# Kernel optimization log

Hardware: AMD Instinct MI355X
Metric: run time of the kernel (lower is better)

The kernel has to match this reference:

```python
import jax, jax.numpy as jnp
import numpy as np

HIDDEN = 1024
TILE = 128


def setup_inputs() -> dict:
    key = jax.random.key(0)
    ks = jax.random.split(key, 9)
    B, S, D = 2, 4096, HIDDEN
    s = 1.0 / np.sqrt(D)
    return {
        "batch": jax.random.normal(ks[0], (B, S, D), jnp.float32),
        "Wq": jax.random.normal(ks[1], (D, D), jnp.float32) * s,
        "bq": jax.random.normal(ks[2], (D,), jnp.float32) * 0.01,
        "Wk": jax.random.normal(ks[3], (D, D), jnp.float32) * s,
        "bk": jax.random.normal(ks[4], (D,), jnp.float32) * 0.01,
        "Wv": jax.random.normal(ks[5], (D, D), jnp.float32) * s,
        "bv": jax.random.normal(ks[6], (D,), jnp.float32) * 0.01,
        "Wo": jax.random.normal(ks[7], (D, D), jnp.float32) * s,
        "bo": jax.random.normal(ks[8], (D,), jnp.float32) * 0.01,
    }


def reference(batch, Wq, bq, Wk, bk, Wv, bv, Wo, bo):
    B, S, D = batch.shape
    scale = 1.0 / np.sqrt(D)
    T = S // TILE  # seq_len chosen divisible by tile size

    # Projections (nn.Linear: x @ W.T + b)
    q = batch @ Wq.T + bq
    k = batch @ Wk.T + bk
    v = batch @ Wv.T + bv

    # Tile K/V along the sequence axis: [B, T, TILE, D]
    k_t = k.reshape(B, T, TILE, D)
    v_t = v.reshape(B, T, TILE, D)

    # Per-tile scores and per-tile softmax (NOT a global softmax —
    # faithful to the module, which normalizes within each kv tile).
    scores = jnp.einsum("bqd,btkd->btqk", q, k_t) * scale  # [B, T, S, TILE]
    w = jax.nn.softmax(scores, axis=-1)

    # Sum of per-tile attention outputs over kv tiles
    out = jnp.einsum("btqk,btkd->bqd", w, v_t)  # [B, S, D]

    # Normalizing factor: sum of per-tile softmax weights (== T analytically,
    # computed explicitly to match the original math bit-for-bit in spirit)
    norm = w.sum(axis=-1).sum(axis=1)[..., None]  # [B, S, 1]
    out = out / (norm + 1e-6)

    return out @ Wo.T + bo
```

## Files before the change

kernel.cpp:

```cpp
#include <hip/hip_runtime.h>


#define D_ 1024
#define S_ 4096
#define B_ 2

typedef unsigned short u16;
typedef float f32x4 __attribute__((ext_vector_type(4)));
typedef float float4v __attribute__((ext_vector_type(4)));
typedef __bf16 bf16x8 __attribute__((ext_vector_type(8)));
typedef unsigned short us8 __attribute__((ext_vector_type(8)));

static __device__ __forceinline__ u16 f2bf(float f) {
    unsigned int u = __builtin_bit_cast(unsigned int, f);
    u += 0x7FFFu + ((u >> 16) & 1u);
    return (u16)(u >> 16);
}

static __device__ __forceinline__ void gld16(const u16* g, u16* l) {
    __builtin_amdgcn_global_load_lds(
        (const __attribute__((address_space(1))) void*)g,
        (__attribute__((address_space(3))) void*)l, 16, 0, 0);
}

static __device__ __forceinline__ void xcd_map(int& bx, int& by) {
    const int gx = gridDim.x, gy = gridDim.y;
    int lin = blockIdx.x + blockIdx.y * gx;
    int ry = gy >> 3;
    int idx = lin >> 3;
    int q = idx / ry;
    bx = q;
    by = (lin & 7) * ry + (idx - q * ry);
}

__global__ void cast_kernel(const float* __restrict__ in, u16* __restrict__ out, int n8) {
    int i = blockIdx.x * blockDim.x + threadIdx.x;
    int stride = gridDim.x * blockDim.x;
    for (; i < n8; i += stride) {
        const float4v* p = (const float4v*)in + 2 * (size_t)i;
        float4v a = p[0], b = p[1];
        us8 o;
        o[0] = f2bf(a[0]); o[1] = f2bf(a[1]); o[2] = f2bf(a[2]); o[3] = f2bf(a[3]);
        o[4] = f2bf(b[0]); o[5] = f2bf(b[1]); o[6] = f2bf(b[2]); o[7] = f2bf(b[3]);
        *((us8*)out + i) = o;
    }
}

__global__ void cast4_kernel(const float* __restrict__ w0, const float* __restrict__ w1,
                             const float* __restrict__ w2, const float* __restrict__ w3,
                             u16* __restrict__ out, int n8per) {
    const float* srcs[4] = {w0, w1, w2, w3};
    const float* in = srcs[blockIdx.y];
    u16* o = out + (size_t)blockIdx.y * (size_t)n8per * 8;
    int i = blockIdx.x * blockDim.x + threadIdx.x;
    int stride = gridDim.x * blockDim.x;
    for (; i < n8per; i += stride) {
        const float4v* p = (const float4v*)in + 2 * (size_t)i;
        float4v a = p[0], b = p[1];
        us8 v;
        v[0] = f2bf(a[0]); v[1] = f2bf(a[1]); v[2] = f2bf(a[2]); v[3] = f2bf(a[3]);
        v[4] = f2bf(b[0]); v[5] = f2bf(b[1]); v[6] = f2bf(b[2]); v[7] = f2bf(b[3]);
        *((us8*)o + i) = v;
    }
}

__global__ void concat_bias(const float* __restrict__ b0, const float* __restrict__ b1,
                            const float* __restrict__ b2, float* __restrict__ out) {
    int i = blockIdx.x * 256 + threadIdx.x;
    const float* s = (i < 1024) ? b0 : ((i < 2048) ? b1 : b2);
    out[i] = s[i & 1023];
}

__global__ void transpose_v(const u16* __restrict__ V, u16* __restrict__ Vt, int ldv) {
    __shared__ u16 t[64][72];
    const int tid = threadIdx.x;
    const int d0 = blockIdx.x * 64;
    const int s0 = blockIdx.y * 64;
    const u16* Vb = V + (size_t)blockIdx.z * ((size_t)S_ * ldv);
    u16* Vtb = Vt + (size_t)blockIdx.z * ((size_t)D_ * S_);
#pragma unroll
    for (int it = 0; it < 2; it++) {
        int idx = it * 256 + tid;
        int row = idx >> 3;
        int ch = idx & 7;
        us8 v = *(const us8*)&Vb[(size_t)(s0 + row) * ldv + d0 + ch * 8];
        *(us8*)&t[row][ch * 8] = v;
    }
    __syncthreads();
#pragma unroll
    for (int it = 0; it < 2; it++) {
        int idx = it * 256 + tid;
        int jj = idx >> 3;
        int ch = idx & 7;
        us8 v;
#pragma unroll
        for (int e = 0; e < 8; e++) v[e] = t[ch * 8 + e][jj];
        *(us8*)&Vtb[(size_t)(d0 + jj) * S_ + s0 + ch * 8] = v;
    }
}

template <int EPI>
__global__ __launch_bounds__(256, 2) void gemm_bt(
    const u16* __restrict__ A, const u16* __restrict__ B, void* __restrict__ Cv,
    const float* __restrict__ bias, int K, int lda, int ldb, int ldc,
    long sA, long sB, long sC, float scale)
{
    __shared__ u16 lA[128 * 32];
    __shared__ u16 lB[128 * 32];
    const int tid = threadIdx.x;
    const int lane = tid & 63;
    const int wid = tid >> 6;
    const int wr = wid >> 1, wc = wid & 1;
    const int z = blockIdx.z;
    A += (size_t)z * sA;
    B += (size_t)z * sB;
    int bx, by;
    xcd_map(bx, by);
    const int m0 = by * 128;
    const int n0 = bx * 128;

    f32x4 acc[4][4];
#pragma unroll
    for (int i = 0; i < 4; i++)
#pragma unroll
        for (int j = 0; j < 4; j++)
#pragma unroll
            for (int r = 0; r < 4; r++) acc[i][j][r] = 0.0f;

    const int ar = lane & 15;
    const int ak = (lane >> 4) * 8;
    const int srow = tid >> 2;
    const int scol = (tid & 3) * 8;
    const u16* ga = A + (size_t)(m0 + srow) * lda + scol;
    const u16* gb = B + (size_t)(n0 + srow) * ldb + scol;

    for (int k0 = 0; k0 < K; k0 += 32) {
        gld16(ga + k0, &lA[tid * 8]);
        gld16(ga + k0 + (size_t)64 * lda, &lA[2048 + tid * 8]);
        gld16(gb + k0, &lB[tid * 8]);
        gld16(gb + k0 + (size_t)64 * ldb, &lB[2048 + tid * 8]);
        __syncthreads();
        bf16x8 afr[4], bfr[4];
#pragma unroll
        for (int mi = 0; mi < 4; mi++)
            afr[mi] = *(const bf16x8*)&lA[(wr * 64 + mi * 16 + ar) * 32 + ak];
#pragma unroll
        for (int ni = 0; ni < 4; ni++)
            bfr[ni] = *(const bf16x8*)&lB[(wc * 64 + ni * 16 + ar) * 32 + ak];
#pragma unroll
        for (int mi = 0; mi < 4; mi++)
#pragma unroll
            for (int ni = 0; ni < 4; ni++)
                acc[mi][ni] = __builtin_amdgcn_mfma_f32_16x16x32_bf16(
                    afr[mi], bfr[ni], acc[mi][ni], 0, 0, 0);
        __syncthreads();
    }

    const int rr = (lane >> 4) * 4;
    const int cc = lane & 15;
#pragma unroll
    for (int mi = 0; mi < 4; mi++) {
#pragma unroll
        for (int ni = 0; ni < 4; ni++) {
            const int col = n0 + wc * 64 + ni * 16 + cc;
            const int rowb = m0 + wr * 64 + mi * 16 + rr;
            if constexpr (EPI == 0) {
                u16* C = (u16*)Cv + (size_t)z * sC;
                const float bv = bias[col];
#pragma unroll
                for (int r = 0; r < 4; r++)
                    C[(size_t)(rowb + r) * ldc + col] = f2bf(acc[mi][ni][r] + bv);
            } else if constexpr (EPI == 1) {
                u16* C = (u16*)Cv + (size_t)z * sC;
#pragma unroll
                for (int r = 0; r < 4; r++)
                    C[(size_t)(rowb + r) * ldc + col] = f2bf(acc[mi][ni][r] * scale);
            } else {
                float* C = (float*)Cv + (size_t)z * sC;
                const float bv = bias[col];
#pragma unroll
                for (int r = 0; r < 4; r++)
                    C[(size_t)(rowb + r) * ldc + col] = acc[mi][ni][r] + bv;
            }
        }
    }
}

__global__ __launch_bounds__(256, 2) void gemm_scores(
    const u16* __restrict__ Q, const u16* __restrict__ Kmat, u16* __restrict__ W,
    int K, int lda, int ldb, int ldc, long sQ, long sK, long sW)
{
    __shared__ u16 lA[128 * 32];
    __shared__ u16 lB[128 * 32];
    const int tid = threadIdx.x;
    const int lane = tid & 63;
    const int wid = tid >> 6;
    const int z = blockIdx.z;
    const u16* Aq = Q + (size_t)z * sQ;
    const u16* Bk = Kmat + (size_t)z * sK;
    int bx, by;
    xcd_map(bx, by);
    const int m0 = by * 128;
    const int n0 = bx * 128;

    f32x4 acc[2][8];
#pragma unroll
    for (int i = 0; i < 2; i++)
#pragma unroll
        for (int j = 0; j < 8; j++)
#pragma unroll
            for (int r = 0; r < 4; r++) acc[i][j][r] = 0.0f;

    const int ar = lane & 15;
    const int ak = (lane >> 4) * 8;
    const int srow = tid >> 2;
    const int scol = (tid & 3) * 8;
    const u16* ga = Aq + (size_t)(m0 + srow) * lda + scol;
    const u16* gb = Bk + (size_t)(n0 + srow) * ldb + scol;

    for (int k0 = 0; k0 < K; k0 += 32) {
        gld16(ga + k0, &lA[tid * 8]);
        gld16(ga + k0 + (size_t)64 * lda, &lA[2048 + tid * 8]);
        gld16(gb + k0, &lB[tid * 8]);
        gld16(gb + k0 + (size_t)64 * ldb, &lB[2048 + tid * 8]);
        __syncthreads();
        bf16x8 afr[2], bfr[8];
#pragma unroll
        for (int mi = 0; mi < 2; mi++)
            afr[mi] = *(const bf16x8*)&lA[(wid * 32 + mi * 16 + ar) * 32 + ak];
#pragma unroll
        for (int ni = 0; ni < 8; ni++)
            bfr[ni] = *(const bf16x8*)&lB[(ni * 16 + ar) * 32 + ak];
#pragma unroll
        for (int mi = 0; mi < 2; mi++)
#pragma unroll
            for (int ni = 0; ni < 8; ni++)
                acc[mi][ni] = __builtin_amdgcn_mfma_f32_16x16x32_bf16(
                    afr[mi], bfr[ni], acc[mi][ni], 0, 0, 0);
        __syncthreads();
    }

    const float SL = 0.03125f * 1.44269504088896341f;
    const int g4 = (lane >> 4) * 4;
    const int cc = lane & 15;
    u16* Wp = W + (size_t)z * sW;
#pragma unroll
    for (int mi = 0; mi < 2; mi++) {
#pragma unroll
        for (int r = 0; r < 4; r++) {
            float m = acc[mi][0][r];
#pragma unroll
            for (int ni = 1; ni < 8; ni++) m = fmaxf(m, acc[mi][ni][r]);
            m = fmaxf(m, __shfl_xor(m, 1));
            m = fmaxf(m, __shfl_xor(m, 2));
            m = fmaxf(m, __shfl_xor(m, 4));
            m = fmaxf(m, __shfl_xor(m, 8));
            float e[8], s = 0.0f;
#pragma unroll
            for (int ni = 0; ni < 8; ni++) {
                e[ni] = exp2f((acc[mi][ni][r] - m) * SL);
                s += e[ni];
            }
            s += __shfl_xor(s, 1);
            s += __shfl_xor(s, 2);
            s += __shfl_xor(s, 4);
            s += __shfl_xor(s, 8);
            const float inv = 1.0f / s;
            const int row = m0 + wid * 32 + mi * 16 + g4 + r;
#pragma unroll
            for (int ni = 0; ni < 8; ni++)
                Wp[(size_t)row * ldc + n0 + ni * 16 + cc] = f2bf(e[ni] * inv);
        }
    }
}

extern "C" void kernel_launch(void* const* d_in, const int* in_sizes, int n_in,
                              void* d_out, int out_size, void* d_ws, size_t ws_size,
                              hipStream_t stream)
{
    const float* X  = (const float*)d_in[0];
    const float* Wq = (const float*)d_in[1];
    const float* bq = (const float*)d_in[2];
    const float* Wk = (const float*)d_in[3];
    const float* bk = (const float*)d_in[4];
    const float* Wv = (const float*)d_in[5];
    const float* bv = (const float*)d_in[6];
    const float* Wo = (const float*)d_in[7];
    const float* bo = (const float*)d_in[8];
    float* OUT = (float*)d_out;

    u16* ws = (u16*)d_ws;
    const size_t NTOK = (size_t)B_ * S_;
    const size_t XSZ = NTOK * D_;
    u16* Xb   = ws;
    u16* QKVb = Xb + XSZ;
    u16* Vt   = QKVb + NTOK * (size_t)(3 * D_);
    u16* Wqb  = Vt + XSZ;
    u16* Wsm  = Wqb + (size_t)4 * D_ * D_;
    float* bqkv = (float*)(Wsm + (size_t)B_ * S_ * S_);
    u16* Ob   = Xb;

    u16* Qp = QKVb;
    u16* Kp = QKVb + D_;
    u16* Vp = QKVb + 2 * D_;
    const int ldqkv = 3 * D_;

    cast_kernel<<<dim3(2048), dim3(256), 0, stream>>>(X, Xb, (int)(XSZ / 8));
    cast4_kernel<<<dim3(512, 4), dim3(256), 0, stream>>>(Wq, Wk, Wv, Wo, Wqb,
                                                         (int)((size_t)D_ * D_ / 8));
    concat_bias<<<dim3(12), dim3(256), 0, stream>>>(bq, bk, bv, bqkv);

    gemm_bt<0><<<dim3(3 * D_ / 128, NTOK / 128, 1), 256, 0, stream>>>(
        Xb, Wqb, QKVb, bqkv, D_, D_, D_, ldqkv, 0, 0, 0, 1.0f);

    transpose_v<<<dim3(D_ / 64, S_ / 64, B_), 256, 0, stream>>>(Vp, Vt, ldqkv);

    gemm_scores<<<dim3(S_ / 128, S_ / 128, B_), 256, 0, stream>>>(
        Qp, Kp, Wsm, D_, ldqkv, ldqkv, S_,
        (long)S_ * ldqkv, (long)S_ * ldqkv, (long)S_ * S_);

    gemm_bt<1><<<dim3(D_ / 128, S_ / 128, B_), 256, 0, stream>>>(
        Wsm, Vt, Ob, nullptr, S_, S_, S_, D_,
        (long)S_ * S_, (long)D_ * S_, (long)S_ * D_, 1.0f / (32.0f + 1e-6f));

    gemm_bt<2><<<dim3(D_ / 128, NTOK / 128, 1), 256, 0, stream>>>(
        Ob, Wqb + (size_t)3 * D_ * D_, OUT, bo, D_, D_, D_, D_, 0, 0, 0, 1.0f);
}
```

Before: 405.1 us.

## Replace GEMMs with 8-wave 256-wide tiles using a 4-stage async LDS pipeline

All GEMMs move onto one templated kernel with 512 threads, 256-column output tiles and a 4-deep ring of LDS buffers. Global-to-LDS loads are issued three k-steps ahead and gated by explicit vmcnt waits instead of full __syncthreads. The kernel also XOR-swizzles the LDS layout to avoid bank conflicts and raises wave priority around the MFMA blocks. The score GEMM now uses 256x256 tiles, so the per-128-column softmax reduces across wave pairs through shared memory. The larger LDS footprint and one block per CU reduce occupancy, and the hand-tuned waitcnt counts make correctness depend on the exact number of outstanding loads.

After: 406.4 us. No clear change (+0.3%).

```diff
diff --git a/kernel.cpp b/kernel.cpp
--- a/kernel.cpp
+++ b/kernel.cpp
@@ -21,6 +21,15 @@
     __builtin_amdgcn_global_load_lds(
         (const __attribute__((address_space(1))) void*)g,
         (__attribute__((address_space(3))) void*)l, 16, 0, 0);
+}
+
+template <int N>
+static __device__ __forceinline__ void waitv() {
+    if constexpr (N == 0)      asm volatile("s_waitcnt vmcnt(0)" ::: "memory");
+    else if constexpr (N == 3) asm volatile("s_waitcnt vmcnt(3)" ::: "memory");
+    else if constexpr (N == 4) asm volatile("s_waitcnt vmcnt(4)" ::: "memory");
+    else if constexpr (N == 6) asm volatile("s_waitcnt vmcnt(6)" ::: "memory");
+    else if constexpr (N == 8) asm volatile("s_waitcnt vmcnt(8)" ::: "memory");
 }
 
 static __device__ __forceinline__ void xcd_map(int& bx, int& by) {
@@ -99,177 +108,203 @@
     }
 }
 
-template <int EPI>
-__global__ __launch_bounds__(256, 2) void gemm_bt(
+template <int BM, int EPI>
+__global__ __launch_bounds__(512, 1) void gemm8(
     const u16* __restrict__ A, const u16* __restrict__ B, void* __restrict__ Cv,
     const float* __restrict__ bias, int K, int lda, int ldb, int ldc,
     long sA, long sB, long sC, float scale)
 {
-    __shared__ u16 lA[128 * 32];
-    __shared__ u16 lB[128 * 32];
+    constexpr int MI = BM / 32;
+    constexpr int MH = MI / 2;
+    constexpr int LPT_A = BM / 128;
+    constexpr int LPT = LPT_A + 2;
+
+    __shared__ u16 lA[4][BM * 32];
+    __shared__ u16 lB[4][256 * 32];
+    __shared__ float sred[2][8][128];
+
     const int tid = threadIdx.x;
     const int lane = tid & 63;
     const int wid = tid >> 6;
-    const int wr = wid >> 1, wc = wid & 1;
+    const int wr = wid >> 2;
+    const int wc = wid & 3;
+    const int ar = lane & 15;
+    const int sl = lane >> 4;
     const int z = blockIdx.z;
     A += (size_t)z * sA;
     B += (size_t)z * sB;
     int bx, by;
     xcd_map(bx, by);
-    const int m0 = by * 128;
-    const int n0 = bx * 128;
-
-    f32x4 acc[4][4];
-#pragma unroll
-    for (int i = 0; i < 4; i++)
+    const int m0 = by * BM;
+    const int n0 = bx * 256;
+    const int NT = K >> 5;
+
+    f32x4 acc[MI][4];
+#pragma unroll
+    for (int i = 0; i < MI; i++)
 #pragma unroll
         for (int j = 0; j < 4; j++)
 #pragma unroll
             for (int r = 0; r < 4; r++) acc[i][j][r] = 0.0f;
 
-    const int ar = lane & 15;
-    const int ak = (lane >> 4) * 8;
-    const int srow = tid >> 2;
-    const int scol = (tid & 3) * 8;
-    const u16* ga = A + (size_t)(m0 + srow) * lda + scol;
-    const u16* gb = B + (size_t)(n0 + srow) * ldb + scol;
-
-    for (int k0 = 0; k0 < K; k0 += 32) {
-        gld16(ga + k0, &lA[tid * 8]);
-        gld16(ga + k0 + (size_t)64 * lda, &lA[2048 + tid * 8]);
-        gld16(gb + k0, &lB[tid * 8]);
-        gld16(gb + k0 + (size_t)64 * ldb, &lB[2048 + tid * 8]);
-        __syncthreads();
-        bf16x8 afr[4], bfr[4];
-#pragma unroll
-        for (int mi = 0; mi < 4; mi++)
-            afr[mi] = *(const bf16x8*)&lA[(wr * 64 + mi * 16 + ar) * 32 + ak];
-#pragma unroll
-        for (int ni = 0; ni < 4; ni++)
-            bfr[ni] = *(const bf16x8*)&lB[(wc * 64 + ni * 16 + ar) * 32 + ak];
-#pragma unroll
-        for (int mi = 0; mi < 4; mi++)
+    auto stageA = [&](int t) {
+        const int k0 = t << 5;
+        u16* dst = &lA[t & 3][0];
+#pragma unroll
+        for (int j = 0; j < LPT_A; j++) {
+            int u = wid * (BM >> 1) + j * 64 + lane;
+            int row = u >> 2, ps = u & 3;
+            int ls = ps ^ ((row >> 1) & 3);
+            gld16(A + (size_t)(m0 + row) * lda + k0 + ls * 8, dst + u * 8);
+        }
+    };
+    auto stageB = [&](int t) {
+        const int k0 = t << 5;
+        u16* dst = &lB[t & 3][0];
+#pragma unroll
+        for (int j = 0; j < 2; j++) {
+            int u = wid * 128 + j * 64 + lane;
+            int row = u >> 2, ps = u & 3;
+            int ls = ps ^ ((row >> 1) & 3);
+            gld16(B + (size_t)(n0 + row) * ldb + k0 + ls * 8, dst + u * 8);
+        }
+    };
+    auto rdA = [&](int buf, int mi) -> bf16x8 {
+        int R = wr * (BM / 2) + mi * 16 + ar;
+        int ps = sl ^ ((R >> 1) & 3);
+        return *(const bf16x8*)&lA[buf][R * 32 + ps * 8];
+    };
+    auto rdB = [&](int buf, int ni) -> bf16x8 {
+        int R = wc * 64 + ni * 16 + ar;
+        int ps = sl ^ ((R >> 1) & 3);
+        return *(const bf16x8*)&lB[buf][R * 32 + ps * 8];
+    };
+
+    stageA(0); stageB(0);
+    stageA(1); stageB(1);
+    stageA(2); stageB(2);
+
+    for (int t = 0; t < NT; ++t) {
+        const int ahead = NT - 1 - t;
+        if (ahead >= 2)      waitv<2 * LPT>();
+        else if (ahead == 1) waitv<LPT>();
+        else                 waitv<0>();
+        __builtin_amdgcn_s_barrier();
+
+        const int buf = t & 3;
+        bf16x8 bfr[4];
+#pragma unroll
+        for (int ni = 0; ni < 4; ni++) bfr[ni] = rdB(buf, ni);
+        bf16x8 afr[MH];
+#pragma unroll
+        for (int mi = 0; mi < MH; mi++) afr[mi] = rdA(buf, mi);
+        if (t + 3 < NT) stageA(t + 3);
+        asm volatile("s_waitcnt lgkmcnt(0)" ::: "memory");
+        __builtin_amdgcn_sched_barrier(0);
+        __builtin_amdgcn_s_setprio(1);
+#pragma unroll
+        for (int mi = 0; mi < MH; mi++)
 #pragma unroll
             for (int ni = 0; ni < 4; ni++)
                 acc[mi][ni] = __builtin_amdgcn_mfma_f32_16x16x32_bf16(
                     afr[mi], bfr[ni], acc[mi][ni], 0, 0, 0);
+        __builtin_amdgcn_s_setprio(0);
+        __builtin_amdgcn_s_barrier();
+
+        bf16x8 afr2[MH];
+#pragma unroll
+        for (int mi = 0; mi < MH; mi++) afr2[mi] = rdA(buf, MH + mi);
+        if (t + 3 < NT) stageB(t + 3);
+        asm volatile("s_waitcnt lgkmcnt(0)" ::: "memory");
+        __builtin_amdgcn_sched_barrier(0);
+        __builtin_amdgcn_s_setprio(1);
+#pragma unroll
+        for (int mi = 0; mi < MH; mi++)
+#pragma unroll
+            for (int ni = 0; ni < 4; ni++)
+                acc[MH + mi][ni] = __builtin_amdgcn_mfma_f32_16x16x32_bf16(
+                    afr2[mi], bfr[ni], acc[MH + mi][ni], 0, 0, 0);
+        __builtin_amdgcn_s_setprio(0);
+    }
+
+    if constexpr (EPI == 3) {
+        const float SL = 0.03125f * 1.44269504088896341f;
+#pragma unroll
+        for (int mi = 0; mi < MI; mi++) {
+#pragma unroll
+            for (int r = 0; r < 4; r++) {
+                float m = acc[mi][0][r];
+#pragma unroll
+                for (int ni = 1; ni < 4; ni++) m = fmaxf(m, acc[mi][ni][r]);
+                m = fmaxf(m, __shfl_xor(m, 1));
+                m = fmaxf(m, __shfl_xor(m, 2));
+                m = fmaxf(m, __shfl_xor(m, 4));
+                m = fmaxf(m, __shfl_xor(m, 8));
+                if (ar == 0) sred[0][wid][mi * 16 + sl * 4 + r] = m;
+            }
+        }
         __syncthreads();
-    }
-
-    const int rr = (lane >> 4) * 4;
-    const int cc = lane & 15;
-#pragma unroll
-    for (int mi = 0; mi < 4; mi++) {
-#pragma unroll
-        for (int ni = 0; ni < 4; ni++) {
-            const int col = n0 + wc * 64 + ni * 16 + cc;
-            const int rowb = m0 + wr * 64 + mi * 16 + rr;
-            if constexpr (EPI == 0) {
-                u16* C = (u16*)Cv + (size_t)z * sC;
-                const float bv = bias[col];
-#pragma unroll
-                for (int r = 0; r < 4; r++)
-                    C[(size_t)(rowb + r) * ldc + col] = f2bf(acc[mi][ni][r] + bv);
-            } else if constexpr (EPI == 1) {
-                u16* C = (u16*)Cv + (size_t)z * sC;
-#pragma unroll
-                for (int r = 0; r < 4; r++)
-                    C[(size_t)(rowb + r) * ldc + col] = f2bf(acc[mi][ni][r] * scale);
-            } else {
-                float* C = (float*)Cv + (size_t)z * sC;
-                const float bv = bias[col];
-#pragma unroll
-                for (int r = 0; r < 4; r++)
-                    C[(size_t)(rowb + r) * ldc + col] = acc[mi][ni][r] + bv;
+#pragma unroll
+        for (int mi = 0; mi < MI; mi++) {
+#pragma unroll
+            for (int r = 0; r < 4; r++) {
+                const int rl = mi * 16 + sl * 4 + r;
+                const float mc = fmaxf(sred[0][wid][rl], sred[0][wid ^ 1][rl]);
+                float s = 0.0f;
+#pragma unroll
+                for (int ni = 0; ni < 4; ni++) {
+                    float e = exp2f((acc[mi][ni][r] - mc) * SL);
+                    acc[mi][ni][r] = e;
+                    s += e;
+                }
+                s += __shfl_xor(s, 1);
+                s += __shfl_xor(s, 2);
+                s += __shfl_xor(s, 4);
+                s += __shfl_xor(s, 8);
+                if (ar == 0) sred[1][wid][rl] = s;
             }
         }
-    }
-}
-
-__global__ __launch_bounds__(256, 2) void gemm_scores(
-    const u16* __restrict__ Q, const u16* __restrict__ Kmat, u16* __restrict__ W,
-    int K, int lda, int ldb, int ldc, long sQ, long sK, long sW)
-{
-    __shared__ u16 lA[128 * 32];
-    __shared__ u16 lB[128 * 32];
-    const int tid = threadIdx.x;
-    const int lane = tid & 63;
-    const int wid = tid >> 6;
-    const int z = blockIdx.z;
-    const u16* Aq = Q + (size_t)z * sQ;
-    const u16* Bk = Kmat + (size_t)z * sK;
-    int bx, by;
-    xcd_map(bx, by);
-    const int m0 = by * 128;
-    const int n0 = bx * 128;
-
-    f32x4 acc[2][8];
-#pragma unroll
-    for (int i = 0; i < 2; i++)
-#pragma unroll
-        for (int j = 0; j < 8; j++)
-#pragma unroll
-            for (int r = 0; r < 4; r++) acc[i][j][r] = 0.0f;
-
-    const int ar = lane & 15;
-    const int ak = (lane >> 4) * 8;
-    const int srow = tid >> 2;
-    const int scol = (tid & 3) * 8;
-    const u16* ga = Aq + (size_t)(m0 + srow) * lda + scol;
-    const u16* gb = Bk + (size_t)(n0 + srow) * ldb + scol;
-
-    for (int k0 = 0; k0 < K; k0 += 32) {
-        gld16(ga + k0, &lA[tid * 8]);
-        gld16(ga + k0 + (size_t)64 * lda, &lA[2048 + tid * 8]);
-        gld16(gb + k0, &lB[tid * 8]);
-        gld16(gb + k0 + (size_t)64 * ldb, &lB[2048 + tid * 8]);
         __syncthreads();
-        bf16x8 afr[2], bfr[8];
-#pragma unroll
-        for (int mi = 0; mi < 2; mi++)
-            afr[mi] = *(const bf16x8*)&lA[(wid * 32 + mi * 16 + ar) * 32 + ak];
-#pragma unroll
-        for (int ni = 0; ni < 8; ni++)
-            bfr[ni] = *(const bf16x8*)&lB[(ni * 16 + ar) * 32 + ak];
-#pragma unroll
-        for (int mi = 0; mi < 2; mi++)
-#pragma unroll
-            for (int ni = 0; ni < 8; ni++)
-                acc[mi][ni] = __builtin_amdgcn_mfma_f32_16x16x32_bf16(
-                    afr[mi], bfr[ni], acc[mi][ni], 0, 0, 0);
-        __syncthreads();
-    }
-
-    const float SL = 0.03125f * 1.44269504088896341f;
-    const int g4 = (lane >> 4) * 4;
-    const int cc = lane & 15;
-    u16* Wp = W + (size_t)z * sW;
-#pragma unroll
-    for (int mi = 0; mi < 2; mi++) {
-#pragma unroll
-        for (int r = 0; r < 4; r++) {
-            float m = acc[mi][0][r];
-#pragma unroll
-            for (int ni = 1; ni < 8; ni++) m = fmaxf(m, acc[mi][ni][r]);
-            m = fmaxf(m, __shfl_xor(m, 1));
-            m = fmaxf(m, __shfl_xor(m, 2));
-            m = fmaxf(m, __shfl_xor(m, 4));
-            m = fmaxf(m, __shfl_xor(m, 8));
-            float e[8], s = 0.0f;
-#pragma unroll
-            for (int ni = 0; ni < 8; ni++) {
-                e[ni] = exp2f((acc[mi][ni][r] - m) * SL);
-                s += e[ni];
+        u16* C = (u16*)Cv + (size_t)z * sC;
+#pragma unroll
+        for (int mi = 0; mi < MI; mi++) {
+#pragma unroll
+            for (int r = 0; r < 4; r++) {
+                const int rl = mi * 16 + sl * 4 + r;
+                const float inv = 1.0f / (sred[1][wid][rl] + sred[1][wid ^ 1][rl]);
+                const int row = m0 + wr * (BM / 2) + rl;
+#pragma unroll
+                for (int ni = 0; ni < 4; ni++)
+                    C[(size_t)row * ldc + n0 + wc * 64 + ni * 16 + ar] =
+                        f2bf(acc[mi][ni][r] * inv);
             }
-            s += __shfl_xor(s, 1);
-            s += __shfl_xor(s, 2);
-            s += __shfl_xor(s, 4);
-            s += __shfl_xor(s, 8);
-            const float inv = 1.0f / s;
-            const int row = m0 + wid * 32 + mi * 16 + g4 + r;
-#pragma unroll
-            for (int ni = 0; ni < 8; ni++)
-                Wp[(size_t)row * ldc + n0 + ni * 16 + cc] = f2bf(e[ni] * inv);
+        }
+    } else {
+#pragma unroll
+        for (int mi = 0; mi < MI; mi++) {
+#pragma unroll
+            for (int ni = 0; ni < 4; ni++) {
+                const int col = n0 + wc * 64 + ni * 16 + ar;
+                const int rowb = m0 + wr * (BM / 2) + mi * 16 + sl * 4;
+                if constexpr (EPI == 0) {
+                    u16* C = (u16*)Cv + (size_t)z * sC;
+                    const float bv = bias[col];
+#pragma unroll
+                    for (int r = 0; r < 4; r++)
+                        C[(size_t)(rowb + r) * ldc + col] = f2bf(acc[mi][ni][r] + bv);
+                } else if constexpr (EPI == 1) {
+                    u16* C = (u16*)Cv + (size_t)z * sC;
+#pragma unroll
+                    for (int r = 0; r < 4; r++)
+                        C[(size_t)(rowb + r) * ldc + col] = f2bf(acc[mi][ni][r] * scale);
+                } else {
+                    float* C = (float*)Cv + (size_t)z * sC;
+                    const float bv = bias[col];
+#pragma unroll
+                    for (int r = 0; r < 4; r++)
+                        C[(size_t)(rowb + r) * ldc + col] = acc[mi][ni][r] + bv;
+                }
+            }
         }
     }
 }
@@ -310,19 +345,19 @@
                                                          (int)((size_t)D_ * D_ / 8));
     concat_bias<<<dim3(12), dim3(256), 0, stream>>>(bq, bk, bv, bqkv);
 
-    gemm_bt<0><<<dim3(3 * D_ / 128, NTOK / 128, 1), 256, 0, stream>>>(
+    gemm8<128, 0><<<dim3(3 * D_ / 256, NTOK / 128, 1), 512, 0, stream>>>(
         Xb, Wqb, QKVb, bqkv, D_, D_, D_, ldqkv, 0, 0, 0, 1.0f);
 
     transpose_v<<<dim3(D_ / 64, S_ / 64, B_), 256, 0, stream>>>(Vp, Vt, ldqkv);
 
-    gemm_scores<<<dim3(S_ / 128, S_ / 128, B_), 256, 0, stream>>>(
-        Qp, Kp, Wsm, D_, ldqkv, ldqkv, S_,
-        (long)S_ * ldqkv, (long)S_ * ldqkv, (long)S_ * S_);
-
-    gemm_bt<1><<<dim3(D_ / 128, S_ / 128, B_), 256, 0, stream>>>(
+    gemm8<256, 3><<<dim3(S_ / 256, S_ / 256, B_), 512, 0, stream>>>(
+        Qp, Kp, Wsm, nullptr, D_, ldqkv, ldqkv, S_,
+        (long)S_ * ldqkv, (long)S_ * ldqkv, (long)S_ * S_, 1.0f);
+
+    gemm8<128, 1><<<dim3(D_ / 256, S_ / 128, B_), 512, 0, stream>>>(
         Wsm, Vt, Ob, nullptr, S_, S_, S_, D_,
         (long)S_ * S_, (long)D_ * S_, (long)S_ * D_, 1.0f / (32.0f + 1e-6f));
 
-    gemm_bt<2><<<dim3(D_ / 128, NTOK / 128, 1), 256, 0, stream>>>(
+    gemm8<128, 2><<<dim3(D_ / 256, NTOK / 128, 1), 512, 0, stream>>>(
         Ob, Wqb + (size_t)3 * D_ * D_, OUT, bo, D_, D_, D_, D_, 0, 0, 0, 1.0f);
 }
```
